# Optimization experiments

Measured on AMD Instinct MI355X. Metric: run time of the kernel, lower is better.

The kernel has to match this reference:

```python
import jax, jax.numpy as jnp
import numpy as np

N_NODES = 100000
N_EDGES = 1600000
N_IN = 32
N_OUT = 32


def setup_inputs() -> dict:
    key = jax.random.key(0)
    ks = jax.random.split(key, 10)
    s = 0.05  # weight init scale
    return {
        'in_vc': jax.random.normal(ks[0], (N_NODES, N_IN), jnp.float32),
        'in_ve': jax.random.normal(ks[1], (N_EDGES, N_IN), jnp.float32),
        'src': jax.random.randint(ks[2], (N_EDGES,), 0, N_NODES),
        'dst': jax.random.randint(ks[3], (N_EDGES,), 0, N_NODES),
        'Wm1': jax.random.normal(ks[4], (3 * N_IN, 3 * N_OUT), jnp.float32) * s,
        'bm1': jnp.zeros((3 * N_OUT,), jnp.float32),
        'Wm2': jax.random.normal(ks[5], (3 * N_OUT, 4 * N_OUT + 1), jnp.float32) * s,
        'bm2': jnp.zeros((4 * N_OUT + 1,), jnp.float32),
        'Wr': jax.random.normal(ks[6], (4 * N_OUT + N_IN, N_OUT), jnp.float32) * s,
        'br': jnp.zeros((N_OUT,), jnp.float32),
        'We': jax.random.normal(ks[7], (4 * N_OUT + N_IN, N_OUT), jnp.float32) * s,
        'be': jnp.zeros((N_OUT,), jnp.float32),
    }


def reference(in_vc, in_ve, src, dst, Wm1, bm1, Wm2, bm2, Wr, br, We, be):
    n_out = N_OUT
    n_nodes = in_vc.shape[0]
    # --- edge message MLP with sigmoid gate ---
    x = jnp.concatenate([in_vc[src], in_vc[dst], in_ve], axis=1)  # [E, 3*n_in]
    h = jax.nn.relu(x @ Wm1 + bm1)
    y = h @ Wm2 + bm2                                             # [E, 4*n_out+1]
    k = jax.nn.sigmoid(y[:, :1])                                  # [E, 1]
    f = y[:, 1:] * k                                              # gated messages [E, 4*n_out]
    f1, f2, f3, f4 = jnp.split(f, 4, axis=1)
    # --- four scatter reductions onto destination nodes ---
    deg = jax.ops.segment_sum(jnp.ones((f1.shape[0],), f1.dtype), dst, num_segments=n_nodes)
    has_in = (deg > 0)[:, None]
    s1 = jax.ops.segment_sum(f1, dst, num_segments=n_nodes)
    m2 = jax.ops.segment_max(f2, dst, num_segments=n_nodes)
    m3 = jax.ops.segment_min(f3, dst, num_segments=n_nodes)
    m4 = jax.ops.segment_sum(f4, dst, num_segments=n_nodes) / jnp.maximum(deg, 1.0)[:, None]
    # DGL leaves nodes with no incoming edges at 0
    m2 = jnp.where(has_in, m2, 0.0)
    m3 = jnp.where(has_in, m3, 0.0)
    # --- node update MLP ---
    node_x = jnp.concatenate([in_vc, s1, m2, m3, m4], axis=1)     # [N, n_in+4*n_out]
    out_vc = node_x @ Wr + br
    # --- edge output MLP ---
    edge_x = jnp.concatenate([f1, f2, f3, f4, in_ve], axis=1)     # [E, 4*n_out+n_in]
    out_ve = edge_x @ We + be
    return (out_vc, out_ve)
```

## Files before the change

### kernel.cpp

```cpp
#include <hip/hip_runtime.h>
#include <cstdint>
#include <cstddef>

#define N_NODES 100000
#define N_EDGES 1600000

#define O_S1   0u
#define O_M4S  3200000u
#define O_M2K  6400000u
#define O_DEG  9600000u
#define O_M3K  9700000u
#define O_WC   12900000u
#define O_C0   12903072u
#define WS_ELEMS 12903104u
#define WS_BYTES ((size_t)WS_ELEMS * 4u)

#define O2_DEG   0u
#define O2_OFF   100000u
#define O2_CUR   200004u
#define O2_EIDX  300004u
#define O2_WC    1900004u
#define O2_C0    1903076u
#define O2_F     1903108u
#define WS2_ELEMS (1903108u + 204800000u)
#define WS2_BYTES ((size_t)WS2_ELEMS * 4u)

__device__ __forceinline__ unsigned fkey(float v){
  unsigned b = __float_as_uint(v);
  return (b & 0x80000000u) ? ~b : (b | 0x80000000u);
}
__device__ __forceinline__ float fdec(unsigned u){
  unsigned b = (u & 0x80000000u) ? (u & 0x7fffffffu) : ~u;
  return __uint_as_float(b);
}

template<int NJ>
__device__ __forceinline__ void accN(float xv, const float* __restrict__ w, float* acc){
  #pragma unroll
  for (int j = 0; j < NJ; j++) acc[j] = fmaf(xv, w[j], acc[j]);
}

__global__ __launch_bounds__(256) void gsmp_make_wc(
    const float* __restrict__ Wm2, const float* __restrict__ bm2,
    const float* __restrict__ We, float* __restrict__ Wc, float* __restrict__ c0)
{
  int t = blockIdx.x * 256 + threadIdx.x;
  if (t < 96 * 32) {
    int k = t >> 5, j = t & 31;
    float s = 0.f;
    for (int i = 0; i < 128; i++) s = fmaf(Wm2[k * 129 + 1 + i], We[i * 32 + j], s);
    Wc[t] = s;
  } else if (t < 96 * 32 + 32) {
    int j = t - 96 * 32;
    float s = 0.f;
    for (int i = 0; i < 128; i++) s = fmaf(bm2[1 + i], We[i * 32 + j], s);
    c0[j] = s;
  }
}

__global__ __launch_bounds__(256) void gsmp_hist(
    const int* __restrict__ dst, unsigned* __restrict__ deg)
{
  int e = blockIdx.x * 256 + threadIdx.x;
  if (e < N_EDGES) atomicAdd(&deg[dst[e]], 1u);
}

__global__ __launch_bounds__(1024) void gsmp_scan(float* __restrict__ wsf)
{
  unsigned* deg = (unsigned*)wsf + O2_DEG;
  unsigned* off = (unsigned*)wsf + O2_OFF;
  unsigned* cur = (unsigned*)wsf + O2_CUR;
  __shared__ unsigned wsum[16];
  __shared__ unsigned carry_s, total_s;
  int t = threadIdx.x;
  int w = t >> 6, lane = t & 63;
  if (t == 0) carry_s = 0u;
  __syncthreads();
  for (int base = 0; base < N_NODES; base += 1024) {
    int n = base + t;
    unsigned v = (n < N_NODES) ? deg[n] : 0u;
    unsigned incl = v;
    #pragma unroll
    for (int o = 1; o < 64; o <<= 1) {
      unsigned u = __shfl_up(incl, o, 64);
      if (lane >= o) incl += u;
    }
    if (lane == 63) wsum[w] = incl;
    __syncthreads();
    if (t < 16) {
      unsigned x = wsum[t], inc = x;
      #pragma unroll
      for (int o = 1; o < 16; o <<= 1) {
        unsigned u = __shfl_up(inc, o, 16);
        if (t >= o) inc += u;
      }
      wsum[t] = inc - x;
      if (t == 15) total_s = inc;
    }
    __syncthreads();
    if (n < N_NODES) {
      unsigned exc = carry_s + wsum[w] + incl - v;
      off[n] = exc;
      cur[n] = exc;
    }
    __syncthreads();
    if (t == 0) carry_s += total_s;
    __syncthreads();
  }
  if (t == 0) off[N_NODES] = carry_s;
}

__global__ __launch_bounds__(256) void gsmp_fill(
    const int* __restrict__ dst, float* __restrict__ wsf)
{
  unsigned* cur  = (unsigned*)wsf + O2_CUR;
  unsigned* eidx = (unsigned*)wsf + O2_EIDX;
  int e = blockIdx.x * 256 + threadIdx.x;
  if (e < N_EDGES) {
    unsigned pos = atomicAdd(&cur[dst[e]], 1u);
    eidx[pos] = (unsigned)e;
  }
}

#define EB 128
#define HLO 56
#define HHI 40
__global__ __launch_bounds__(EB, 3) void gsmp_edge_fast(
    const float* __restrict__ in_vc, const float* __restrict__ in_ve,
    const int* __restrict__ src, const int* __restrict__ dst,
    const float* __restrict__ Wm1, const float* __restrict__ bm1,
    const float* __restrict__ Wm2, const float* __restrict__ bm2,
    const float* __restrict__ We, const float* __restrict__ be,
    float* __restrict__ ws, float* __restrict__ out_ve)
{
  __shared__ float hlds[EB * HHI];
  int e = blockIdx.x * EB + threadIdx.x;
  bool act = e < N_EDGES;
  int e0 = act ? e : 0;
  int sn = src[e0] * 32;
  int dn = dst[e0] * 32;
  size_t eoff = (size_t)e0 * 32;

  const float* base0 = in_vc + sn;
  const float* base1 = in_vc + dn;
  const float* base2 = in_ve + eoff;
  float* myh = hlds + threadIdx.x * HHI;

  {
    float hh[HHI];
    #pragma unroll
    for (int j = 0; j < HHI; j++) hh[j] = bm1[HLO + j];
    #pragma unroll
    for (int r = 0; r < 3; r++) {
      const float* bp = (r == 0) ? base0 : (r == 1) ? base1 : base2;
      const float4* p4 = (const float4*)bp;
      for (int kc = 0; kc < 8; kc++) {
        float4 xq = p4[kc];
        const float* w = Wm1 + (r * 32 + kc * 4) * 96 + HLO;
        accN<HHI>(xq.x, w + 0 * 96, hh);
        accN<HHI>(xq.y, w + 1 * 96, hh);
        accN<HHI>(xq.z, w + 2 * 96, hh);
        accN<HHI>(xq.w, w + 3 * 96, hh);
      }
    }
    #pragma unroll
    for (int j = 0; j < HHI; j += 4) {
      float4 v;
      v.x = fmaxf(hh[j + 0], 0.f); v.y = fmaxf(hh[j + 1], 0.f);
      v.z = fmaxf(hh[j + 2], 0.f); v.w = fmaxf(hh[j + 3], 0.f);
      *(float4*)(myh + j) = v;
    }
  }

  float hl[HLO];
  #pragma unroll
  for (int j = 0; j < HLO; j++) hl[j] = bm1[j];
  #pragma unroll
  for (int r = 0; r < 3; r++) {
    const float* bp = (r == 0) ? base0 : (r == 1) ? base1 : base2;
    const float4* p4 = (const float4*)bp;
    for (int kc = 0; kc < 8; kc++) {
      float4 xq = p4[kc];
      const float* w = Wm1 + (r * 32 + kc * 4) * 96;
      accN<HLO>(xq.x, w + 0 * 96, hl);
      accN<HLO>(xq.y, w + 1 * 96, hl);
      accN<HLO>(xq.z, w + 2 * 96, hl);
      accN<HLO>(xq.w, w + 3 * 96, hl);
    }
  }
  #pragma unroll
  for (int j = 0; j < HLO; j++) hl[j] = fmaxf(hl[j], 0.f);

  const float4* h4 = (const float4*)myh;

  float y0 = bm2[0];
  #pragma unroll
  for (int k = 0; k < HLO; k++) y0 = fmaf(hl[k], Wm2[k * 129], y0);
  for (int kc = 0; kc < HHI / 4; kc++) {
    float4 hq = h4[kc];
    int k = HLO + kc * 4;
    y0 = fmaf(hq.x, Wm2[(k + 0) * 129], y0);
    y0 = fmaf(hq.y, Wm2[(k + 1) * 129], y0);
    y0 = fmaf(hq.z, Wm2[(k + 2) * 129], y0);
    y0 = fmaf(hq.w, Wm2[(k + 3) * 129], y0);
  }
  float gate = 1.f / (1.f + __expf(-y0));

  float* fbuf = ws + O2_F;

  for (int c = 0; c < 4; c++) {
    float f[32];
    #pragma unroll
    for (int j = 0; j < 32; j++) f[j] = bm2[1 + c * 32 + j];
    #pragma unroll
    for (int k = 0; k < HLO; k++)
      accN<32>(hl[k], Wm2 + k * 129 + 1 + c * 32, f);
    for (int kc = 0; kc < HHI / 4; kc++) {
      float4 hq = h4[kc];
      const float* w = Wm2 + (HLO + kc * 4) * 129 + 1 + c * 32;
      accN<32>(hq.x, w + 0 * 129, f);
      accN<32>(hq.y, w + 1 * 129, f);
      accN<32>(hq.z, w + 2 * 129, f);
      accN<32>(hq.w, w + 3 * 129, f);
    }
    #pragma unroll
    for (int j = 0; j < 32; j++) f[j] *= gate;
    if (act) {
      float4* fp = (float4*)(fbuf + (size_t)e * 128 + c * 32);
      #pragma unroll
      for (int jc = 0; jc < 8; jc++) {
        float4 o;
        o.x = f[jc * 4 + 0]; o.y = f[jc * 4 + 1];
        o.z = f[jc * 4 + 2]; o.w = f[jc * 4 + 3];
        fp[jc] = o;
      }
    }
  }

  const float* Wc = ws + O2_WC;
  const float* c0 = ws + O2_C0;
  float ove[32];
  #pragma unroll
  for (int j = 0; j < 32; j++) ove[j] = 0.f;
  #pragma unroll
  for (int k = 0; k < HLO; k++)
    accN<32>(hl[k], Wc + k * 32, ove);
  for (int kc = 0; kc < HHI / 4; kc++) {
    float4 hq = h4[kc];
    const float* w = Wc + (HLO + kc * 4) * 32;
    accN<32>(hq.x, w + 0 * 32, ove);
    accN<32>(hq.y, w + 1 * 32, ove);
    accN<32>(hq.z, w + 2 * 32, ove);
    accN<32>(hq.w, w + 3 * 32, ove);
  }
  #pragma unroll
  for (int j = 0; j < 32; j++) ove[j] = fmaf(gate, ove[j] + c0[j], be[j]);
  {
    const float4* v4 = (const float4*)base2;
    for (int kc = 0; kc < 8; kc++) {
      float4 vq = v4[kc];
      const float* w = We + (128 + kc * 4) * 32;
      accN<32>(vq.x, w + 0 * 32, ove);
      accN<32>(vq.y, w + 1 * 32, ove);
      accN<32>(vq.z, w + 2 * 32, ove);
      accN<32>(vq.w, w + 3 * 32, ove);
    }
  }
  if (act) {
    float4* op = (float4*)(out_ve + eoff);
    #pragma unroll
    for (int jc = 0; jc < 8; jc++) {
      float4 o;
      o.x = ove[jc * 4 + 0]; o.y = ove[jc * 4 + 1];
      o.z = ove[jc * 4 + 2]; o.w = ove[jc * 4 + 3];
      op[jc] = o;
    }
  }
}

__global__ __launch_bounds__(256) void gsmp_node_fast(
    const float* __restrict__ in_vc, const float* __restrict__ Wr,
    const float* __restrict__ br, const float* __restrict__ ws,
    float* __restrict__ out_vc)
{
  __shared__ float xs[8][128];
  int g = threadIdx.x >> 5;
  int j = threadIdx.x & 31;
  int n = blockIdx.x * 8 + g;

  const unsigned* off  = (const unsigned*)ws + O2_OFF;
  const unsigned* eidx = (const unsigned*)ws + O2_EIDX;
  const float* fbuf = ws + O2_F;

  unsigned beg = 0, end = 0;
  if (n < N_NODES) { beg = off[n]; end = off[n + 1]; }

  const float INF = __builtin_huge_valf();
  float s1 = 0.f, m4 = 0.f, m2 = -INF, m3 = INF;
  for (unsigned i = beg; i < end; i++) {
    unsigned e = eidx[i];
    const float* __restrict__ fb = fbuf + (size_t)e * 128;
    s1 += fb[j];
    m2 = fmaxf(m2, fb[32 + j]);
    m3 = fminf(m3, fb[64 + j]);
    m4 += fb[96 + j];
  }
  bool has = end > beg;
  if (!has) { m2 = 0.f; m3 = 0.f; }
  m4 *= has ? (1.f / (float)(end - beg)) : 1.f;

  xs[g][0 * 32 + j] = s1;
  xs[g][1 * 32 + j] = m2;
  xs[g][2 * 32 + j] = m3;
  xs[g][3 * 32 + j] = m4;
  __syncthreads();
  if (n >= N_NODES) return;

  float acc = br[j];
  const float* vcn = in_vc + (size_t)n * 32;
  #pragma unroll 8
  for (int k = 0; k < 32; k++)  acc = fmaf(vcn[k],   Wr[k * 32 + j],        acc);
  const float* xg = xs[g];
  #pragma unroll 8
  for (int k = 0; k < 128; k++) acc = fmaf(xg[k],    Wr[(32 + k) * 32 + j], acc);
  out_vc[(size_t)n * 32 + j] = acc;
}

__global__ __launch_bounds__(EB) void gsmp_edge_kernel(
    const float* __restrict__ in_vc, const float* __restrict__ in_ve,
    const int* __restrict__ src, const int* __restrict__ dst,
    const float* __restrict__ Wm1, const float* __restrict__ bm1,
    const float* __restrict__ Wm2, const float* __restrict__ bm2,
    const float* __restrict__ We, const float* __restrict__ be,
    float* __restrict__ ws, float* __restrict__ out_ve)
{
  __shared__ float hlds[EB * 100];
  int e = blockIdx.x * EB + threadIdx.x;
  bool act = e < N_EDGES;
  int e0 = act ? e : 0;
  int sn = src[e0] * 32;
  int dn = dst[e0] * 32;
  size_t eoff = (size_t)e0 * 32;

  float h[96];
  #pragma unroll
  for (int j = 0; j < 96; j++) h[j] = bm1[j];

  const float* base0 = in_vc + sn;
  const float* base1 = in_vc + dn;
  const float* base2 = in_ve + eoff;
  #pragma unroll
  for (int r = 0; r < 3; r++) {
    const float* bp = (r == 0) ? base0 : (r == 1) ? base1 : base2;
    const float4* p4 = (const float4*)bp;
    for (int kc = 0; kc < 8; kc++) {
      float4 xq = p4[kc];
      const float* w = Wm1 + (r * 32 + kc * 4) * 96;
      accN<96>(xq.x, w + 0 * 96, h);
      accN<96>(xq.y, w + 1 * 96, h);
      accN<96>(xq.z, w + 2 * 96, h);
      accN<96>(xq.w, w + 3 * 96, h);
    }
  }
  float* myh = hlds + threadIdx.x * 100;
  #pragma unroll
  for (int j = 0; j < 96; j += 4) {
    float4 v;
    v.x = fmaxf(h[j + 0], 0.f); v.y = fmaxf(h[j + 1], 0.f);
    v.z = fmaxf(h[j + 2], 0.f); v.w = fmaxf(h[j + 3], 0.f);
    *(float4*)(myh + j) = v;
  }

  const float4* h4 = (const float4*)myh;
  float y0 = bm2[0];
  for (int kc = 0; kc < 24; kc++) {
    float4 hq = h4[kc];
    int k = kc * 4;
    y0 = fmaf(hq.x, Wm2[(k + 0) * 129], y0);
    y0 = fmaf(hq.y, Wm2[(k + 1) * 129], y0);
    y0 = fmaf(hq.z, Wm2[(k + 2) * 129], y0);
    y0 = fmaf(hq.w, Wm2[(k + 3) * 129], y0);
  }
  float gate = 1.f / (1.f + __expf(-y0));

  float* s1  = ws + O_S1;
  float* m4s = ws + O_M4S;
  unsigned* m2k = (unsigned*)ws + O_M2K;
  unsigned* m3k = (unsigned*)ws + O_M3K;
  unsigned* deg = (unsigned*)ws + O_DEG;

  for (int c = 0; c < 4; c++) {
    float f[32];
    #pragma unroll
    for (int j = 0; j < 32; j++) f[j] = bm2[1 + c * 32 + j];
    for (int kc = 0; kc < 24; kc++) {
      float4 hq = h4[kc];
      const float* w = Wm2 + (kc * 4) * 129 + 1 + c * 32;
      accN<32>(hq.x, w + 0 * 129, f);
      accN<32>(hq.y, w + 1 * 129, f);
      accN<32>(hq.z, w + 2 * 129, f);
      accN<32>(hq.w, w + 3 * 129, f);
    }
    #pragma unroll
    for (int j = 0; j < 32; j++) f[j] *= gate;
    if (act) {
      if (c == 0) {
        #pragma unroll
        for (int j = 0; j < 32; j++) atomicAdd(&s1[dn + j], f[j]);
      } else if (c == 1) {
        #pragma unroll
        for (int j = 0; j < 32; j++) atomicMax(&m2k[dn + j], fkey(f[j]));
      } else if (c == 2) {
        #pragma unroll
        for (int j = 0; j < 32; j++) atomicMin(&m3k[dn + j], fkey(f[j]));
      } else {
        #pragma unroll
        for (int j = 0; j < 32; j++) atomicAdd(&m4s[dn + j], f[j]);
      }
    }
  }
  if (act) atomicAdd(&deg[dn >> 5], 1u);

  const float* Wc = ws + O_WC;
  const float* c0 = ws + O_C0;
  float ove[32];
  #pragma unroll
  for (int j = 0; j < 32; j++) ove[j] = 0.f;
  for (int kc = 0; kc < 24; kc++) {
    float4 hq = h4[kc];
    const float* w = Wc + (kc * 4) * 32;
    accN<32>(hq.x, w + 0 * 32, ove);
    accN<32>(hq.y, w + 1 * 32, ove);
    accN<32>(hq.z, w + 2 * 32, ove);
    accN<32>(hq.w, w + 3 * 32, ove);
  }
  #pragma unroll
  for (int j = 0; j < 32; j++) ove[j] = fmaf(gate, ove[j] + c0[j], be[j]);
  {
    const float4* v4 = (const float4*)base2;
    for (int kc = 0; kc < 8; kc++) {
      float4 vq = v4[kc];
      const float* w = We + (128 + kc * 4) * 32;
      accN<32>(vq.x, w + 0 * 32, ove);
      accN<32>(vq.y, w + 1 * 32, ove);
      accN<32>(vq.z, w + 2 * 32, ove);
      accN<32>(vq.w, w + 3 * 32, ove);
    }
  }
  if (act) {
    float4* op = (float4*)(out_ve + eoff);
    #pragma unroll
    for (int jc = 0; jc < 8; jc++) {
      float4 o;
      o.x = ove[jc * 4 + 0]; o.y = ove[jc * 4 + 1];
      o.z = ove[jc * 4 + 2]; o.w = ove[jc * 4 + 3];
      op[jc] = o;
    }
  }
}

__global__ __launch_bounds__(256) void gsmp_node_kernel(
    const float* __restrict__ in_vc, const float* __restrict__ Wr,
    const float* __restrict__ br, const float* __restrict__ ws,
    float* __restrict__ out_vc)
{
  int n = blockIdx.x * 256 + threadIdx.x;
  if (n >= N_NODES) return;
  const float* s1  = ws + O_S1;
  const float* m4s = ws + O_M4S;
  const unsigned* m2k = (const unsigned*)ws + O_M2K;
  const unsigned* m3k = (const unsigned*)ws + O_M3K;
  const unsigned* deg = (const unsigned*)ws + O_DEG;

  unsigned d = deg[n];
  bool has = d > 0;
  float invd = 1.f / (float)(has ? d : 1u);
  int nb = n * 32;

  float acc[32];
  #pragma unroll
  for (int j = 0; j < 32; j++) acc[j] = br[j];

  for (int k = 0; k < 32; k++) accN<32>(in_vc[nb + k],                 Wr + (0   + k) * 32, acc);
  for (int k = 0; k < 32; k++) accN<32>(s1[nb + k],                    Wr + (32  + k) * 32, acc);
  for (int k = 0; k < 32; k++) accN<32>(has ? fdec(m2k[nb + k]) : 0.f, Wr + (64  + k) * 32, acc);
  for (int k = 0; k < 32; k++) accN<32>(has ? fdec(m3k[nb + k]) : 0.f, Wr + (96  + k) * 32, acc);
  for (int k = 0; k < 32; k++) accN<32>(m4s[nb + k] * invd,            Wr + (128 + k) * 32, acc);

  float4* op = (float4*)(out_vc + (size_t)nb);
  #pragma unroll
  for (int jc = 0; jc < 8; jc++) {
    float4 o;
    o.x = acc[jc * 4 + 0]; o.y = acc[jc * 4 + 1];
    o.z = acc[jc * 4 + 2]; o.w = acc[jc * 4 + 3];
    op[jc] = o;
  }
}

extern "C" void kernel_launch(void* const* d_in, const int* in_sizes, int n_in,
                              void* d_out, int out_size, void* d_ws, size_t ws_size,
                              hipStream_t stream) {
  const float* in_vc = (const float*)d_in[0];
  const float* in_ve = (const float*)d_in[1];
  const int*   src   = (const int*)d_in[2];
  const int*   dst   = (const int*)d_in[3];
  const float* Wm1   = (const float*)d_in[4];
  const float* bm1   = (const float*)d_in[5];
  const float* Wm2   = (const float*)d_in[6];
  const float* bm2   = (const float*)d_in[7];
  const float* Wr    = (const float*)d_in[8];
  const float* br    = (const float*)d_in[9];
  const float* We    = (const float*)d_in[10];
  const float* be    = (const float*)d_in[11];

  float* ws     = (float*)d_ws;
  float* out_vc = (float*)d_out;
  float* out_ve = out_vc + (size_t)N_NODES * 32;

  if (ws_size >= WS2_BYTES) {
    hipMemsetAsync(ws + O2_DEG, 0, (size_t)N_NODES * 4, stream);
    gsmp_make_wc<<<13, 256, 0, stream>>>(Wm2, bm2, We, ws + O2_WC, ws + O2_C0);
    gsmp_hist<<<(N_EDGES + 255) / 256, 256, 0, stream>>>(dst, (unsigned*)ws + O2_DEG);
    gsmp_scan<<<1, 1024, 0, stream>>>(ws);
    gsmp_fill<<<(N_EDGES + 255) / 256, 256, 0, stream>>>(dst, ws);
    gsmp_edge_fast<<<N_EDGES / EB, EB, 0, stream>>>(
        in_vc, in_ve, src, dst, Wm1, bm1, Wm2, bm2, We, be, ws, out_ve);
    gsmp_node_fast<<<(N_NODES + 7) / 8, 256, 0, stream>>>(in_vc, Wr, br, ws, out_vc);
  } else if (ws_size >= WS_BYTES) {
    hipMemsetAsync(ws + O_S1, 0, (size_t)(O_M3K - O_S1) * 4, stream);
    hipMemsetAsync(ws + O_M3K, 0xFF, (size_t)(N_NODES * 32) * 4, stream);
    gsmp_make_wc<<<13, 256, 0, stream>>>(Wm2, bm2, We, ws + O_WC, ws + O_C0);
    gsmp_edge_kernel<<<N_EDGES / EB, EB, 0, stream>>>(
        in_vc, in_ve, src, dst, Wm1, bm1, Wm2, bm2, We, be, ws, out_ve);
    gsmp_node_kernel<<<(N_NODES + 255) / 256, 256, 0, stream>>>(
        in_vc, Wr, br, ws, out_vc);
  }
}
```

Measured before the change: 2.937 ms.

## Split edge MLP into two LDS-weight kernels with four threads per edge

Replaces the fused single-thread-per-edge kernel with two kernels. The first computes the hidden layer and sigmoid gate using Wm1 staged in LDS and four threads per edge, then writes h and the gate to workspace. The second reads h back, computes the gated messages and the edge output using Wm2 and the folded Wc staged in LDS. The aim is to cut register pressure and serve weights from LDS. The cost is an extra 96-float-per-edge round trip through global memory and a much larger workspace, and this path runs only if the harness provides that workspace.

```diff
diff --git a/kernel.cpp b/kernel.cpp
--- a/kernel.cpp
+++ b/kernel.cpp
@@ -25,6 +25,11 @@
 #define WS2_ELEMS (1903108u + 204800000u)
 #define WS2_BYTES ((size_t)WS2_ELEMS * 4u)
 
+#define O2_H   206703108u
+#define O2_G   360303108u
+#define WS3_ELEMS 361903108u
+#define WS3_BYTES ((size_t)WS3_ELEMS * 4u)
+
 __device__ __forceinline__ unsigned fkey(float v){
   unsigned b = __float_as_uint(v);
   return (b & 0x80000000u) ? ~b : (b | 0x80000000u);
@@ -35,7 +40,7 @@
 }
 
 template<int NJ>
-__device__ __forceinline__ void accN(float xv, const float* __restrict__ w, float* acc){
+__device__ __forceinline__ void accN(float xv, const float* w, float* acc){
   #pragma unroll
   for (int j = 0; j < NJ; j++) acc[j] = fmaf(xv, w[j], acc[j]);
 }
@@ -122,6 +127,213 @@
   }
 }
 
+__global__ __launch_bounds__(512, 4) void gsmp_edge_h(
+    const float* __restrict__ in_vc, const float* __restrict__ in_ve,
+    const int* __restrict__ src, const int* __restrict__ dst,
+    const float* __restrict__ Wm1, const float* __restrict__ bm1,
+    const float* __restrict__ Wm2, const float* __restrict__ bm2,
+    float* __restrict__ ws)
+{
+  __shared__ float wlds[96 * 96];
+  __shared__ float col0[96];
+  __shared__ float b1[96];
+  int tid = threadIdx.x;
+  for (int i = tid; i < 96 * 96; i += 512) wlds[i] = Wm1[i];
+  if (tid < 96) { col0[tid] = Wm2[tid * 129]; b1[tid] = bm1[tid]; }
+  __syncthreads();
+
+  int eg = tid >> 2, q = tid & 3;
+  int e = blockIdx.x * 128 + eg;
+  int s32 = src[e] * 32, d32 = dst[e] * 32;
+  size_t eoff = (size_t)e * 32;
+
+  float h[24];
+  #pragma unroll
+  for (int j = 0; j < 24; j++) h[j] = b1[24 * q + j];
+
+  const float* seg0 = in_vc + s32;
+  const float* seg1 = in_vc + d32;
+  const float* seg2 = in_ve + eoff;
+  #pragma unroll
+  for (int c = 0; c < 6; c++) {
+    const float* bp = (c < 2) ? seg0 : (c < 4) ? seg1 : seg2;
+    const float4* p4 = (const float4*)bp + (c & 1) * 4;
+    float4 x0 = p4[0], x1 = p4[1], x2 = p4[2], x3 = p4[3];
+    float xs[16] = {x0.x, x0.y, x0.z, x0.w, x1.x, x1.y, x1.z, x1.w,
+                    x2.x, x2.y, x2.z, x2.w, x3.x, x3.y, x3.z, x3.w};
+    int kb = c * 16;
+    #pragma unroll
+    for (int kk = 0; kk < 16; kk++) {
+      const float* w = wlds + (kb + kk) * 96 + 24 * q;
+      accN<24>(xs[kk], w, h);
+    }
+  }
+
+  float y = 0.f;
+  #pragma unroll
+  for (int j = 0; j < 24; j++) {
+    h[j] = fmaxf(h[j], 0.f);
+    y = fmaf(h[j], col0[24 * q + j], y);
+  }
+  y += __shfl_xor(y, 1, 64);
+  y += __shfl_xor(y, 2, 64);
+  y += bm2[0];
+  float gate = 1.f / (1.f + __expf(-y));
+
+  float* hp = ws + O2_H + (size_t)e * 96 + 24 * q;
+  #pragma unroll
+  for (int jc = 0; jc < 6; jc++) {
+    float4 o;
+    o.x = h[jc * 4 + 0]; o.y = h[jc * 4 + 1];
+    o.z = h[jc * 4 + 2]; o.w = h[jc * 4 + 3];
+    ((float4*)hp)[jc] = o;
+  }
+  if (q == 0) ws[O2_G + e] = gate;
+}
+
+__global__ __launch_bounds__(512, 4) void gsmp_edge_f(
+    const float* __restrict__ in_ve,
+    const float* __restrict__ Wm2, const float* __restrict__ bm2,
+    const float* __restrict__ We, const float* __restrict__ be,
+    float* __restrict__ ws, float* __restrict__ out_ve)
+{
+  __shared__ float wlds[96 * 144];
+  __shared__ float wc[96 * 32];
+  __shared__ float wet[32 * 32];
+  __shared__ float fb[128];
+  __shared__ float c0s[32];
+  __shared__ float bes[32];
+  int tid = threadIdx.x;
+  for (int i = tid; i < 96 * 128; i += 512) {
+    int k = i >> 7, col = i & 127;
+    wlds[k * 144 + (col >> 5) * 36 + (col & 31)] = Wm2[k * 129 + 1 + col];
+  }
+  for (int i = tid; i < 96 * 32; i += 512) wc[i] = ws[O2_WC + i];
+  for (int i = tid; i < 32 * 32; i += 512) wet[i] = We[(128 + (i >> 5)) * 32 + (i & 31)];
+  if (tid < 128) fb[tid] = bm2[1 + tid];
+  if (tid < 32) { c0s[tid] = ws[O2_C0 + tid]; bes[tid] = be[tid]; }
+  __syncthreads();
+
+  int eg = tid >> 2, q = tid & 3;
+  int e = blockIdx.x * 128 + eg;
+  const float4* hp4 = (const float4*)(ws + O2_H + (size_t)e * 96);
+  float gate = ws[O2_G + e];
+
+  float f[32];
+  #pragma unroll
+  for (int j = 0; j < 32; j++) f[j] = 0.f;
+  #pragma unroll
+  for (int c = 0; c < 6; c++) {
+    float4 h0 = hp4[c * 4 + 0], h1 = hp4[c * 4 + 1];
+    float4 h2 = hp4[c * 4 + 2], h3 = hp4[c * 4 + 3];
+    float hs[16] = {h0.x, h0.y, h0.z, h0.w, h1.x, h1.y, h1.z, h1.w,
+                    h2.x, h2.y, h2.z, h2.w, h3.x, h3.y, h3.z, h3.w};
+    int kb = c * 16;
+    #pragma unroll
+    for (int kk = 0; kk < 16; kk++) {
+      const float* w = wlds + (kb + kk) * 144 + q * 36;
+      accN<32>(hs[kk], w, f);
+    }
+  }
+  #pragma unroll
+  for (int j = 0; j < 32; j++) f[j] = gate * (f[j] + fb[32 * q + j]);
+  {
+    float4* fp = (float4*)(ws + O2_F + (size_t)e * 128 + 32 * q);
+    #pragma unroll
+    for (int jc = 0; jc < 8; jc++) {
+      float4 o;
+      o.x = f[jc * 4 + 0]; o.y = f[jc * 4 + 1];
+      o.z = f[jc * 4 + 2]; o.w = f[jc * 4 + 3];
+      fp[jc] = o;
+    }
+  }
+
+  float ov[8];
+  #pragma unroll
+  for (int j = 0; j < 8; j++) ov[j] = 0.f;
+  #pragma unroll
+  for (int c = 0; c < 6; c++) {
+    float4 h0 = hp4[c * 4 + 0], h1 = hp4[c * 4 + 1];
+    float4 h2 = hp4[c * 4 + 2], h3 = hp4[c * 4 + 3];
+    float hs[16] = {h0.x, h0.y, h0.z, h0.w, h1.x, h1.y, h1.z, h1.w,
+                    h2.x, h2.y, h2.z, h2.w, h3.x, h3.y, h3.z, h3.w};
+    int kb = c * 16;
+    #pragma unroll
+    for (int kk = 0; kk < 16; kk++)
+      accN<8>(hs[kk], wc + (kb + kk) * 32 + 8 * q, ov);
+  }
+  #pragma unroll
+  for (int j = 0; j < 8; j++) ov[j] = gate * (ov[j] + c0s[8 * q + j]);
+  {
+    const float4* v4 = (const float4*)(in_ve + (size_t)e * 32);
+    #pragma unroll
+    for (int kc = 0; kc < 8; kc++) {
+      float4 vq = v4[kc];
+      accN<8>(vq.x, wet + (kc * 4 + 0) * 32 + 8 * q, ov);
+      accN<8>(vq.y, wet + (kc * 4 + 1) * 32 + 8 * q, ov);
+      accN<8>(vq.z, wet + (kc * 4 + 2) * 32 + 8 * q, ov);
+      accN<8>(vq.w, wet + (kc * 4 + 3) * 32 + 8 * q, ov);
+    }
+  }
+  #pragma unroll
+  for (int j = 0; j < 8; j++) ov[j] += bes[8 * q + j];
+  {
+    float4* op = (float4*)(out_ve + (size_t)e * 32 + 8 * q);
+    float4 o0, o1;
+    o0.x = ov[0]; o0.y = ov[1]; o0.z = ov[2]; o0.w = ov[3];
+    o1.x = ov[4]; o1.y = ov[5]; o1.z = ov[6]; o1.w = ov[7];
+    op[0] = o0; op[1] = o1;
+  }
+}
+
+__global__ __launch_bounds__(256) void gsmp_node_fast(
+    const float* __restrict__ in_vc, const float* __restrict__ Wr,
+    const float* __restrict__ br, const float* __restrict__ ws,
+    float* __restrict__ out_vc)
+{
+  __shared__ float xs[8][128];
+  int g = threadIdx.x >> 5;
+  int j = threadIdx.x & 31;
+  int n = blockIdx.x * 8 + g;
+
+  const unsigned* off  = (const unsigned*)ws + O2_OFF;
+  const unsigned* eidx = (const unsigned*)ws + O2_EIDX;
+  const float* fbuf = ws + O2_F;
+
+  unsigned beg = 0, end = 0;
+  if (n < N_NODES) { beg = off[n]; end = off[n + 1]; }
+
+  const float INF = __builtin_huge_valf();
+  float s1 = 0.f, m4 = 0.f, m2 = -INF, m3 = INF;
+  for (unsigned i = beg; i < end; i++) {
+    unsigned e = eidx[i];
+    const float* __restrict__ fb = fbuf + (size_t)e * 128;
+    s1 += fb[j];
+    m2 = fmaxf(m2, fb[32 + j]);
+    m3 = fminf(m3, fb[64 + j]);
+    m4 += fb[96 + j];
+  }
+  bool has = end > beg;
+  if (!has) { m2 = 0.f; m3 = 0.f; }
+  m4 *= has ? (1.f / (float)(end - beg)) : 1.f;
+
+  xs[g][0 * 32 + j] = s1;
+  xs[g][1 * 32 + j] = m2;
+  xs[g][2 * 32 + j] = m3;
+  xs[g][3 * 32 + j] = m4;
+  __syncthreads();
+  if (n >= N_NODES) return;
+
+  float acc = br[j];
+  const float* vcn = in_vc + (size_t)n * 32;
+  #pragma unroll 8
+  for (int k = 0; k < 32; k++)  acc = fmaf(vcn[k], Wr[k * 32 + j], acc);
+  const float* xg = xs[g];
+  #pragma unroll 8
+  for (int k = 0; k < 128; k++) acc = fmaf(xg[k], Wr[(32 + k) * 32 + j], acc);
+  out_vc[(size_t)n * 32 + j] = acc;
+}
+
 #define EB 128
 #define HLO 56
 #define HHI 40
@@ -276,54 +488,6 @@
       op[jc] = o;
     }
   }
-}
-
-__global__ __launch_bounds__(256) void gsmp_node_fast(
-    const float* __restrict__ in_vc, const float* __restrict__ Wr,
-    const float* __restrict__ br, const float* __restrict__ ws,
-    float* __restrict__ out_vc)
-{
-  __shared__ float xs[8][128];
-  int g = threadIdx.x >> 5;
-  int j = threadIdx.x & 31;
-  int n = blockIdx.x * 8 + g;
-
-  const unsigned* off  = (const unsigned*)ws + O2_OFF;
-  const unsigned* eidx = (const unsigned*)ws + O2_EIDX;
-  const float* fbuf = ws + O2_F;
-
-  unsigned beg = 0, end = 0;
-  if (n < N_NODES) { beg = off[n]; end = off[n + 1]; }
-
-  const float INF = __builtin_huge_valf();
-  float s1 = 0.f, m4 = 0.f, m2 = -INF, m3 = INF;
-  for (unsigned i = beg; i < end; i++) {
-    unsigned e = eidx[i];
-    const float* __restrict__ fb = fbuf + (size_t)e * 128;
-    s1 += fb[j];
-    m2 = fmaxf(m2, fb[32 + j]);
-    m3 = fminf(m3, fb[64 + j]);
-    m4 += fb[96 + j];
-  }
-  bool has = end > beg;
-  if (!has) { m2 = 0.f; m3 = 0.f; }
-  m4 *= has ? (1.f / (float)(end - beg)) : 1.f;
-
-  xs[g][0 * 32 + j] = s1;
-  xs[g][1 * 32 + j] = m2;
-  xs[g][2 * 32 + j] = m3;
-  xs[g][3 * 32 + j] = m4;
-  __syncthreads();
-  if (n >= N_NODES) return;
-
-  float acc = br[j];
-  const float* vcn = in_vc + (size_t)n * 32;
-  #pragma unroll 8
-  for (int k = 0; k < 32; k++)  acc = fmaf(vcn[k],   Wr[k * 32 + j],        acc);
-  const float* xg = xs[g];
-  #pragma unroll 8
-  for (int k = 0; k < 128; k++) acc = fmaf(xg[k],    Wr[(32 + k) * 32 + j], acc);
-  out_vc[(size_t)n * 32 + j] = acc;
 }
 
 __global__ __launch_bounds__(EB) void gsmp_edge_kernel(
@@ -517,7 +681,18 @@
   float* out_vc = (float*)d_out;
   float* out_ve = out_vc + (size_t)N_NODES * 32;
 
-  if (ws_size >= WS2_BYTES) {
+  if (ws_size >= WS3_BYTES) {
+    hipMemsetAsync(ws + O2_DEG, 0, (size_t)N_NODES * 4, stream);
+    gsmp_make_wc<<<13, 256, 0, stream>>>(Wm2, bm2, We, ws + O2_WC, ws + O2_C0);
+    gsmp_hist<<<(N_EDGES + 255) / 256, 256, 0, stream>>>(dst, (unsigned*)ws + O2_DEG);
+    gsmp_scan<<<1, 1024, 0, stream>>>(ws);
+    gsmp_fill<<<(N_EDGES + 255) / 256, 256, 0, stream>>>(dst, ws);
+    gsmp_edge_h<<<N_EDGES / 128, 512, 0, stream>>>(
+        in_vc, in_ve, src, dst, Wm1, bm1, Wm2, bm2, ws);
+    gsmp_edge_f<<<N_EDGES / 128, 512, 0, stream>>>(
+        in_ve, Wm2, bm2, We, be, ws, out_ve);
+    gsmp_node_fast<<<(N_NODES + 7) / 8, 256, 0, stream>>>(in_vc, Wr, br, ws, out_vc);
+  } else if (ws_size >= WS2_BYTES) {
     hipMemsetAsync(ws + O2_DEG, 0, (size_t)N_NODES * 4, stream);
     gsmp_make_wc<<<13, 256, 0, stream>>>(Wm2, bm2, We, ws + O2_WC, ws + O2_C0);
     gsmp_hist<<<(N_EDGES + 255) / 256, 256, 0, stream>>>(dst, (unsigned*)ws + O2_DEG);
```

Measured after the change: 2.958 ms. Within noise of the previous version (+0.7%).
